# Kernel optimization log

Hardware: AMD Instinct MI355X
Metric: run time of the kernel (lower is better)

Reference implementation:

```python
import jax, jax.numpy as jnp
import numpy as np

D_MODEL = 768
N_HEADS = 4
HEAD_DIM = D_MODEL // N_HEADS


def setup_inputs() -> dict:
    key = jax.random.key(0)
    ks = jax.random.split(key, 9)
    B, S = 4, 2048
    scale = 1.0 / np.sqrt(D_MODEL)
    inputs = jax.random.normal(ks[0], (B, S, D_MODEL), dtype=jnp.float32)
    # Linear weights stored as [in, out] for x @ W + b
    Wq = jax.random.normal(ks[1], (D_MODEL, D_MODEL), dtype=jnp.float32) * scale
    bq = jnp.zeros((D_MODEL,), dtype=jnp.float32)
    Wk = jax.random.normal(ks[2], (D_MODEL, D_MODEL), dtype=jnp.float32) * scale
    bk = jnp.zeros((D_MODEL,), dtype=jnp.float32)
    Wv = jax.random.normal(ks[3], (D_MODEL, D_MODEL), dtype=jnp.float32) * scale
    bv = jnp.zeros((D_MODEL,), dtype=jnp.float32)
    Wo = jax.random.normal(ks[4], (D_MODEL, D_MODEL), dtype=jnp.float32) * scale
    bo = jnp.zeros((D_MODEL,), dtype=jnp.float32)
    return {"inputs": inputs, "Wq": Wq, "bq": bq, "Wk": Wk, "bk": bk,
            "Wv": Wv, "bv": bv, "Wo": Wo, "bo": bo}


def reference(inputs, Wq, bq, Wk, bk, Wv, bv, Wo, bo):
    B, S, _ = inputs.shape
    H, Dh = N_HEADS, HEAD_DIM
    # projections -> [B, H, S, Dh]
    def split_heads(x):
        return x.reshape(B, S, H, Dh).transpose(0, 2, 1, 3)
    Q = split_heads(inputs @ Wq + bq)
    K = split_heads(inputs @ Wk + bk)
    V = split_heads(inputs @ Wv + bv)
    scores = jnp.einsum('bhqd,bhkd->bhqk', Q, K) / jnp.sqrt(jnp.float32(Dh))
    causal = jnp.tril(jnp.ones((S, S), dtype=bool))  # True = keep
    scores = jnp.where(causal, scores, -jnp.inf)
    weights = jax.nn.softmax(scores, axis=-1)
    # dropout is identity in eval mode
    ctx = jnp.einsum('bhqk,bhkd->bhqd', weights, V)
    ctx = ctx.transpose(0, 2, 1, 3).reshape(B, S, H * Dh)
    return ctx @ Wo + bo
```

## Files before the change

### kernel.cpp

```cpp
#include <hip/hip_runtime.h>
#include <hip/hip_bf16.h>
#include <cstddef>

typedef __attribute__((ext_vector_type(8))) short short8;
typedef __attribute__((ext_vector_type(4))) float f32x4;
typedef __attribute__((ext_vector_type(16))) float f32x16;
typedef __attribute__((ext_vector_type(4))) unsigned short u16x4;

#define D_MODEL 768
#define N_HEADS 4
#define HEAD_DIM 192
#define BATCH 4
#define SEQ 2048
#define M_ROWS (BATCH*SEQ)

__device__ __forceinline__ short f2bf(float f) {
  union { float f; unsigned u; } v; v.f = f;
  unsigned r = v.u + 0x7FFFu + ((v.u >> 16) & 1u);
  return (short)(r >> 16);
}

__device__ __forceinline__ float fexp2(float x) {
  return __builtin_amdgcn_exp2f(x);
}

__device__ __forceinline__ void gl_lds16(const void* g, void* l) {
  __builtin_amdgcn_global_load_lds(
      (const __attribute__((address_space(1))) void*)g,
      (__attribute__((address_space(3))) void*)l, 16, 0, 0);
}

__global__ __launch_bounds__(256) void cast_kernel(const float* __restrict__ src,
                                                   short* __restrict__ dst, int n8) {
  int i = blockIdx.x * 256 + threadIdx.x;
  if (i >= n8) return;
  const float4* s = (const float4*)src;
  float4 a = s[2 * i], b = s[2 * i + 1];
  short8 o;
  o[0] = f2bf(a.x); o[1] = f2bf(a.y); o[2] = f2bf(a.z); o[3] = f2bf(a.w);
  o[4] = f2bf(b.x); o[5] = f2bf(b.y); o[6] = f2bf(b.z); o[7] = f2bf(b.w);
  *(short8*)(dst + (size_t)i * 8) = o;
}

__global__ __launch_bounds__(256) void wtrans(const float* __restrict__ W,
                                              short* __restrict__ Wt) {
  __shared__ float tile[32][33];
  int k0 = blockIdx.x * 32, n0 = blockIdx.y * 32;
  int tc = threadIdx.x & 31, tr = threadIdx.x >> 5;
#pragma unroll
  for (int i = 0; i < 4; i++)
    tile[tr + i * 8][tc] = W[(size_t)(k0 + tr + i * 8) * D_MODEL + n0 + tc];
  __syncthreads();
#pragma unroll
  for (int i = 0; i < 4; i++)
    Wt[(size_t)(n0 + tr + i * 8) * D_MODEL + k0 + tc] = f2bf(tile[tc][tr + i * 8]);
}

__global__ __launch_bounds__(256) void bias_concat(const float* __restrict__ a,
                                                   const float* __restrict__ b,
                                                   const float* __restrict__ c,
                                                   float* __restrict__ dst) {
  int i = blockIdx.x * 256 + threadIdx.x;
  if (i >= 3 * D_MODEL) return;
  float v = i < 768 ? a[i] : (i < 1536 ? b[i - 768] : c[i - 1536]);
  dst[i] = v;
}

template <int MODE>
__global__ __launch_bounds__(256, 4) void gemm_bf16(const short* __restrict__ A,
                                                    const short* __restrict__ Wt,
                                                    const float* __restrict__ bias,
                                                    short* __restrict__ oQ,
                                                    short* __restrict__ oK,
                                                    short* __restrict__ oV,
                                                    float* __restrict__ oF, int N) {
  __shared__ short As[128 * 64];
  __shared__ short Bs[128 * 64];
  const int K = 768;
  const int m0 = blockIdx.x * 128, n0 = blockIdx.y * 128;
  const int t = threadIdx.x, lane = t & 63, w = t >> 6;
  const int wr = w >> 1, wc = w & 1, lr = lane & 15, lg = lane >> 4;

  f32x4 acc[4][4] = {};

  for (int k0 = 0; k0 < K; k0 += 64) {
#pragma unroll
    for (int i = 0; i < 4; i++) {
      int id = w * 4 + i;
      int row = id * 8 + (lane >> 3);
      int cc = (lane & 7) ^ (row & 7);
      gl_lds16(A + (size_t)(m0 + row) * K + k0 + cc * 8, As + id * 512);
      gl_lds16(Wt + (size_t)(n0 + row) * K + k0 + cc * 8, Bs + id * 512);
    }
    __syncthreads();
#pragma unroll
    for (int kb = 0; kb < 2; kb++) {
      short8 a[4], b[4];
#pragma unroll
      for (int m = 0; m < 4; m++) {
        int row = wr * 64 + m * 16 + lr;
        a[m] = *(const short8*)&As[row * 64 + (((kb * 4 + lg) ^ (row & 7)) << 3)];
      }
#pragma unroll
      for (int n = 0; n < 4; n++) {
        int row = wc * 64 + n * 16 + lr;
        b[n] = *(const short8*)&Bs[row * 64 + (((kb * 4 + lg) ^ (row & 7)) << 3)];
      }
#pragma unroll
      for (int m = 0; m < 4; m++)
#pragma unroll
        for (int n = 0; n < 4; n++)
          acc[m][n] = __builtin_amdgcn_mfma_f32_16x16x32_bf16(a[m], b[n], acc[m][n], 0, 0, 0);
    }
    __syncthreads();
  }

  if (MODE == 0) {
#pragma unroll
    for (int m = 0; m < 4; m++)
#pragma unroll
      for (int n = 0; n < 4; n++) {
        int col = n0 + wc * 64 + n * 16 + lr;
        float bv = bias[col];
#pragma unroll
        for (int r = 0; r < 4; r++) {
          int row = m0 + wr * 64 + m * 16 + lg * 4 + r;
          oF[(size_t)row * N + col] = acc[m][n][r] + bv;
        }
      }
  } else {
    const int bb = m0 >> 11;
#pragma unroll
    for (int m = 0; m < 4; m++) {
      int s0 = (m0 & (SEQ - 1)) + wr * 64 + m * 16 + lg * 4;
#pragma unroll
      for (int n = 0; n < 4; n++) {
        int col = n0 + wc * 64 + n * 16 + lr;
        int seg = col / 768;
        int d = col - seg * 768;
        int h = d / HEAD_DIM, dd = d - h * HEAD_DIM;
        int bh = bb * N_HEADS + h;
        float bv = bias[col];
        if (seg < 2) {
          short* dst = seg == 0 ? oQ : oK;
#pragma unroll
          for (int r = 0; r < 4; r++)
            dst[((size_t)bh * SEQ + s0 + r) * HEAD_DIM + dd] = f2bf(acc[m][n][r] + bv);
        } else {
          u16x4 pk;
#pragma unroll
          for (int r = 0; r < 4; r++) pk[r] = (unsigned short)f2bf(acc[m][n][r] + bv);
          *(u16x4*)&oV[((size_t)bh * HEAD_DIM + dd) * SEQ + s0] = pk;
        }
      }
    }
  }
}

__device__ __forceinline__ void stage_kv(const short* Kp, const short* Vp, int kbase,
                                         short* KsB, short* VsB, int w, int lane) {
#pragma unroll
  for (int i = 0; i < 6; i++) {
    int id = w * 6 + i;
    int o16 = id * 64 + lane;
    int row = o16 / 24, cc0 = o16 - row * 24;
    int cc = cc0 ^ (row & 7);
    gl_lds16(Kp + (size_t)(kbase + row) * HEAD_DIM + cc * 8, KsB + id * 512);
  }
#pragma unroll
  for (int i = 0; i < 6; i++) {
    int id = w * 6 + i;
    int o16 = id * 64 + lane;
    int row = o16 >> 3, cc = (o16 & 7) ^ (row & 7);
    gl_lds16(Vp + (size_t)row * SEQ + kbase + cc * 8, VsB + id * 512);
  }
}

__global__ __launch_bounds__(256, 2) void attn_kernel(const short* __restrict__ Q,
                                                      const short* __restrict__ Kg,
                                                      const short* __restrict__ Vt,
                                                      short* __restrict__ ctx) {
  __shared__ short smem[64 * 192 + 192 * 64];
  __shared__ float mlbuf[128];
  short* Ks = smem;
  short* Vs = smem + 64 * 192;
  float* obuf = (float*)smem;

  const int i = blockIdx.x;
  int bh, qt;
  if (i < 256) { bh = i & 15; qt = 31 - (i >> 4); }
  else         { int j = i - 256; bh = j & 15; qt = j >> 4; }

  const int b = bh >> 2, head = bh & 3;
  const short* Qp = Q + (size_t)bh * SEQ * HEAD_DIM;
  const short* Kp = Kg + (size_t)bh * SEQ * HEAD_DIM;
  const short* Vp = Vt + (size_t)bh * HEAD_DIM * SEQ;
  const int t = threadIdx.x, lane = t & 63, w = t >> 6;
  const int wq = w >> 1, wk = w & 1;
  const int l31 = lane & 31, hl = lane >> 5;
  const float scale2 = 0.07216878364870322f * 1.4426950408889634f;

  const int nkb = qt + 1;
  const int q0w = qt * 64 + wq * 32;
  const int qlane = q0w + l31;

  short8 qf[12];
#pragma unroll
  for (int c = 0; c < 12; c++)
    qf[c] = *(const short8*)&Qp[(size_t)qlane * HEAD_DIM + c * 16 + hl * 8];

  f32x16 oacc[6];
#pragma unroll
  for (int d = 0; d < 6; d++) oacc[d] = 0.f;
  float m = -3.0e38f, lsum = 0.f;

  for (int kb = 0; kb < nkb; kb++) {
    const int kbase = kb * 64;
    stage_kv(Kp, Vp, kbase, Ks, Vs, w, lane);
    asm volatile("s_waitcnt vmcnt(0)" ::: "memory");
    __builtin_amdgcn_s_barrier();
    asm volatile("" ::: "memory");

    if (kbase + wk * 32 <= q0w + 31) {
      f32x16 sacc = 0.f;
      const int krow = wk * 32 + l31;
      const int krb = krow * 192;
      const int kswz = (krow & 7) << 3;
      __builtin_amdgcn_s_setprio(1);
#pragma unroll
      for (int c = 0; c < 12; c++) {
        short8 kf = *(const short8*)&Ks[krb + ((c * 16 + hl * 8) ^ kswz)];
        sacc = __builtin_amdgcn_mfma_f32_32x32x16_bf16(kf, qf[c], sacc, 0, 0, 0);
      }
      __builtin_amdgcn_s_setprio(0);

      float s[16];
      const bool need_mask = (kbase + wk * 32 + 31) > q0w;
      const int kb0 = kbase + wk * 32 + 4 * hl;
#pragma unroll
      for (int r = 0; r < 16; r++) {
        float v = sacc[r] * scale2;
        if (need_mask) {
          int kg = kb0 + (r & 3) + 8 * (r >> 2);
          if (kg > qlane) v = -3.0e38f;
        }
        s[r] = v;
      }
      float mx = s[0];
#pragma unroll
      for (int r = 1; r < 16; r++) mx = fmaxf(mx, s[r]);
      mx = fmaxf(mx, __shfl_xor(mx, 32, 64));
      if (!__all(mx <= m + 8.0f)) {
        float mn = fmaxf(m, mx);
        float al = fexp2(m - mn);
        m = mn;
        lsum *= al;
#pragma unroll
        for (int d = 0; d < 6; d++) oacc[d] *= al;
      }
      float pr[16];
      float rs = 0.f;
#pragma unroll
      for (int r = 0; r < 16; r++) {
        pr[r] = fexp2(s[r] - m);
        rs += pr[r];
      }
      rs += __shfl_xor(rs, 32, 64);
      lsum += rs;

      unsigned pk[8], ex[8];
#pragma unroll
      for (int j = 0; j < 8; j++) {
        unsigned r0;
        asm("v_cvt_pk_bf16_f32 %0, %1, %2" : "=v"(r0) : "v"(pr[2 * j]), "v"(pr[2 * j + 1]));
        pk[j] = r0;
      }
#pragma unroll
      for (int j = 0; j < 8; j++) ex[j] = __shfl_xor((int)pk[j], 32, 64);
      union { unsigned u[4]; short8 s8; } f0, f1;
      f0.u[0] = hl ? ex[2] : pk[0];
      f0.u[1] = hl ? ex[3] : pk[1];
      f0.u[2] = hl ? pk[2] : ex[0];
      f0.u[3] = hl ? pk[3] : ex[1];
      f1.u[0] = hl ? ex[6] : pk[4];
      f1.u[1] = hl ? ex[7] : pk[5];
      f1.u[2] = hl ? pk[6] : ex[4];
      f1.u[3] = hl ? pk[7] : ex[5];

      __builtin_amdgcn_s_setprio(1);
#pragma unroll
      for (int db = 0; db < 6; db++) {
        const int vrow = db * 32 + l31;
        const int vrb = vrow * 64;
        const int vswz = (vrow & 7) << 3;
        short8 va = *(const short8*)&Vs[vrb + ((wk * 32 + hl * 8) ^ vswz)];
        oacc[db] = __builtin_amdgcn_mfma_f32_32x32x16_bf16(va, f0.s8, oacc[db], 0, 0, 0);
        short8 vb = *(const short8*)&Vs[vrb + ((wk * 32 + 16 + hl * 8) ^ vswz)];
        oacc[db] = __builtin_amdgcn_mfma_f32_32x32x16_bf16(vb, f1.s8, oacc[db], 0, 0, 0);
      }
      __builtin_amdgcn_s_setprio(0);
    }
    asm volatile("" ::: "memory");
    __builtin_amdgcn_s_barrier();
  }

  __syncthreads();
  if (wk == 1) {
    if (lane < 32) {
      mlbuf[wq * 64 + lane] = m;
      mlbuf[wq * 64 + 32 + lane] = lsum;
    }
#pragma unroll
    for (int db = 0; db < 6; db++)
#pragma unroll
      for (int g = 0; g < 4; g++) {
        int d = db * 32 + 8 * g + 4 * hl;
        f32x4 vv;
        vv[0] = oacc[db][4 * g];
        vv[1] = oacc[db][4 * g + 1];
        vv[2] = oacc[db][4 * g + 2];
        vv[3] = oacc[db][4 * g + 3];
        *(f32x4*)&obuf[(wq * 32 + l31) * 192 + (d ^ ((l31 & 7) << 2))] = vv;
      }
  }
  __syncthreads();
  if (wk == 0) {
    float m1 = mlbuf[wq * 64 + l31];
    float l1 = mlbuf[wq * 64 + 32 + l31];
    float ms = fmaxf(m, m1);
    float a0 = fexp2(m - ms), a1 = fexp2(m1 - ms);
    float lt = lsum * a0 + l1 * a1;
    float rl = 1.0f / lt;
#pragma unroll
    for (int db = 0; db < 6; db++)
#pragma unroll
      for (int g = 0; g < 4; g++) {
        int d = db * 32 + 8 * g + 4 * hl;
        f32x4 rd = *(const f32x4*)&obuf[(wq * 32 + l31) * 192 + (d ^ ((l31 & 7) << 2))];
        u16x4 pkk;
#pragma unroll
        for (int r2 = 0; r2 < 4; r2++) {
          float v = (oacc[db][4 * g + r2] * a0 + rd[r2] * a1) * rl;
          pkk[r2] = (unsigned short)f2bf(v);
        }
        *(u16x4*)&ctx[((size_t)b * SEQ + qlane) * D_MODEL + head * HEAD_DIM + d] = pkk;
      }
  }
}

extern "C" void kernel_launch(void* const* d_in, const int* in_sizes, int n_in,
                              void* d_out, int out_size, void* d_ws, size_t ws_size,
                              hipStream_t stream) {
  const float* X  = (const float*)d_in[0];
  const float* Wq = (const float*)d_in[1];
  const float* bq = (const float*)d_in[2];
  const float* Wk = (const float*)d_in[3];
  const float* bk = (const float*)d_in[4];
  const float* Wv = (const float*)d_in[5];
  const float* bv = (const float*)d_in[6];
  const float* Wo = (const float*)d_in[7];
  const float* bo = (const float*)d_in[8];

  char* ws = (char*)d_ws;
  const size_t XB = (size_t)M_ROWS * D_MODEL * 2;
  const size_t WQKV = (size_t)3 * D_MODEL * D_MODEL * 2;
  const size_t WB = (size_t)D_MODEL * D_MODEL * 2;

  short* Xb    = (short*)(ws);
  short* Wqkvt = (short*)(ws + XB);
  short* Wot   = (short*)(ws + XB + WQKV);
  float* bqkv  = (float*)(ws + XB + WQKV + WB);
  short* Qb    = (short*)(ws + XB + WQKV + WB + 12288);
  short* Kb    = (short*)(ws + XB + WQKV + WB + 12288 + XB);
  short* Vtb   = (short*)(ws + XB + WQKV + WB + 12288 + 2 * XB);
  short* Cb    = (short*)(ws + XB + WQKV + WB + 12288 + 3 * XB);

  const int n8x = M_ROWS * D_MODEL / 8;
  cast_kernel<<<(n8x + 255) / 256, 256, 0, stream>>>(X, Xb, n8x);
  dim3 tg(24, 24);
  wtrans<<<tg, 256, 0, stream>>>(Wq, Wqkvt);
  wtrans<<<tg, 256, 0, stream>>>(Wk, Wqkvt + (size_t)768 * 768);
  wtrans<<<tg, 256, 0, stream>>>(Wv, Wqkvt + (size_t)2 * 768 * 768);
  wtrans<<<tg, 256, 0, stream>>>(Wo, Wot);
  bias_concat<<<9, 256, 0, stream>>>(bq, bk, bv, bqkv);

  gemm_bf16<1><<<dim3(M_ROWS / 128, 2304 / 128), 256, 0, stream>>>(
      Xb, Wqkvt, bqkv, Qb, Kb, Vtb, nullptr, 2304);

  attn_kernel<<<512, 256, 0, stream>>>(Qb, Kb, Vtb, Cb);

  gemm_bf16<0><<<dim3(M_ROWS / 128, 768 / 128), 256, 0, stream>>>(
      Cb, Wot, bo, nullptr, nullptr, nullptr, (float*)d_out, 768);
}
```

Baseline: 144.7 us.

## Prefetch next K/V tile into registers to overlap global loads with compute

Replaces the direct global-to-LDS K/V staging with a register-staged software pipeline. The next tile is loaded into registers while the current tile is computed, then written to LDS at the start of the next iteration. The aim is to hide global memory latency behind the MFMA work instead of waiting on vmcnt(0) each iteration. In exchange it costs 12 extra short8 registers per thread, which may reduce occupancy under launch_bounds(256,2), and it adds explicit LDS writes.

```diff
diff --git a/kernel.cpp b/kernel.cpp
--- a/kernel.cpp
+++ b/kernel.cpp
@@ -157,22 +157,25 @@
   }
 }
 
-__device__ __forceinline__ void stage_kv(const short* Kp, const short* Vp, int kbase,
-                                         short* KsB, short* VsB, int w, int lane) {
+__device__ __forceinline__ void load_kv_regs(const short* Kp, const short* Vp, int kbase,
+                                             int w, int lane, short8* kr, short8* vr) {
 #pragma unroll
   for (int i = 0; i < 6; i++) {
-    int id = w * 6 + i;
-    int o16 = id * 64 + lane;
-    int row = o16 / 24, cc0 = o16 - row * 24;
-    int cc = cc0 ^ (row & 7);
-    gl_lds16(Kp + (size_t)(kbase + row) * HEAD_DIM + cc * 8, KsB + id * 512);
-  }
+    int o16 = (w * 6 + i) * 64 + lane;
+    int row = o16 / 24, cc = (o16 - row * 24) ^ (row & 7);
+    kr[i] = *(const short8*)&Kp[(size_t)(kbase + row) * HEAD_DIM + cc * 8];
+    int vrow = o16 >> 3, vcc = (o16 & 7) ^ (vrow & 7);
+    vr[i] = *(const short8*)&Vp[(size_t)vrow * SEQ + kbase + vcc * 8];
+  }
+}
+
+__device__ __forceinline__ void write_kv_lds(short* Ks, short* Vs, int w, int lane,
+                                             const short8* kr, const short8* vr) {
 #pragma unroll
   for (int i = 0; i < 6; i++) {
-    int id = w * 6 + i;
-    int o16 = id * 64 + lane;
-    int row = o16 >> 3, cc = (o16 & 7) ^ (row & 7);
-    gl_lds16(Vp + (size_t)row * SEQ + kbase + cc * 8, VsB + id * 512);
+    int o16 = (w * 6 + i) * 64 + lane;
+    *(short8*)&Ks[o16 * 8] = kr[i];
+    *(short8*)&Vs[o16 * 8] = vr[i];
   }
 }
 
@@ -214,10 +217,20 @@
   for (int d = 0; d < 6; d++) oacc[d] = 0.f;
   float m = -3.0e38f, lsum = 0.f;
 
+  short8 kr[6], vr[6];
+  load_kv_regs(Kp, Vp, 0, w, lane, kr, vr);
+
   for (int kb = 0; kb < nkb; kb++) {
     const int kbase = kb * 64;
-    stage_kv(Kp, Vp, kbase, Ks, Vs, w, lane);
-    asm volatile("s_waitcnt vmcnt(0)" ::: "memory");
+
+    asm volatile("" ::: "memory");
+    __builtin_amdgcn_s_barrier();
+    asm volatile("" ::: "memory");
+    write_kv_lds(Ks, Vs, w, lane, kr, vr);
+    if (kb + 1 < nkb)
+      load_kv_regs(Kp, Vp, kbase + 64, w, lane, kr, vr);
+    asm volatile("s_waitcnt lgkmcnt(0)" ::: "memory");
+    __builtin_amdgcn_sched_barrier(0);
     __builtin_amdgcn_s_barrier();
     asm volatile("" ::: "memory");
 
@@ -300,8 +313,6 @@
       }
       __builtin_amdgcn_s_setprio(0);
     }
-    asm volatile("" ::: "memory");
-    __builtin_amdgcn_s_barrier();
   }
 
   __syncthreads();
```

New measurement: 176.9 us. 1.22x slower.

## Double-buffer K tiles and overlap V loading with QK^T compute

Applied to the files above, without the earlier changes.

Splits K/V staging so the next K tile is prefetched into a second LDS buffer while the current tile is used. The V load for the current block is issued first, and the QK^T MFMAs plus softmax run before waiting on V. A second wait and barrier is placed before the PV matmul. This is meant to hide global-to-LDS latency behind compute. In exchange, LDS per block grows from 48KB to 72KB and each iteration gains an extra barrier, which may limit occupancy.

```diff
diff --git a/kernel.cpp b/kernel.cpp
--- a/kernel.cpp
+++ b/kernel.cpp
@@ -157,16 +157,19 @@
   }
 }
 
-__device__ __forceinline__ void stage_kv(const short* Kp, const short* Vp, int kbase,
-                                         short* KsB, short* VsB, int w, int lane) {
+__device__ __forceinline__ void stage_K(const short* Kp, int kbase, short* KsB,
+                                        int w, int lane) {
 #pragma unroll
   for (int i = 0; i < 6; i++) {
     int id = w * 6 + i;
     int o16 = id * 64 + lane;
-    int row = o16 / 24, cc0 = o16 - row * 24;
-    int cc = cc0 ^ (row & 7);
+    int row = o16 / 24, cc = (o16 - row * 24) ^ (row & 7);
     gl_lds16(Kp + (size_t)(kbase + row) * HEAD_DIM + cc * 8, KsB + id * 512);
   }
+}
+
+__device__ __forceinline__ void stage_V(const short* Vp, int kbase, short* VsB,
+                                        int w, int lane) {
 #pragma unroll
   for (int i = 0; i < 6; i++) {
     int id = w * 6 + i;
@@ -180,10 +183,11 @@
                                                       const short* __restrict__ Kg,
                                                       const short* __restrict__ Vt,
                                                       short* __restrict__ ctx) {
-  __shared__ short smem[64 * 192 + 192 * 64];
+  __shared__ short smem[2 * 64 * 192 + 192 * 64];
   __shared__ float mlbuf[128];
-  short* Ks = smem;
-  short* Vs = smem + 64 * 192;
+  short* Kbuf0 = smem;
+  short* Kbuf1 = smem + 64 * 192;
+  short* Vs = smem + 2 * 64 * 192;
   float* obuf = (float*)smem;
 
   const int i = blockIdx.x;
@@ -214,14 +218,29 @@
   for (int d = 0; d < 6; d++) oacc[d] = 0.f;
   float m = -3.0e38f, lsum = 0.f;
 
+  stage_K(Kp, 0, Kbuf0, w, lane);
+
   for (int kb = 0; kb < nkb; kb++) {
+    const int cur = kb & 1;
     const int kbase = kb * 64;
-    stage_kv(Kp, Vp, kbase, Ks, Vs, w, lane);
-    asm volatile("s_waitcnt vmcnt(0)" ::: "memory");
+    short* Kc = cur ? Kbuf1 : Kbuf0;
+    const bool has_next = (kb + 1 < nkb);
+
+    stage_V(Vp, kbase, Vs, w, lane);
+    if (has_next) {
+      stage_K(Kp, kbase + 64, cur ? Kbuf0 : Kbuf1, w, lane);
+      asm volatile("s_waitcnt vmcnt(12)" ::: "memory");
+    } else {
+      asm volatile("s_waitcnt vmcnt(6)" ::: "memory");
+    }
     __builtin_amdgcn_s_barrier();
     asm volatile("" ::: "memory");
 
-    if (kbase + wk * 32 <= q0w + 31) {
+    const bool active = (kbase + wk * 32 <= q0w + 31);
+    unsigned pk[8], ex[8];
+    float pr[16];
+
+    if (active) {
       f32x16 sacc = 0.f;
       const int krow = wk * 32 + l31;
       const int krb = krow * 192;
@@ -229,7 +248,7 @@
       __builtin_amdgcn_s_setprio(1);
 #pragma unroll
       for (int c = 0; c < 12; c++) {
-        short8 kf = *(const short8*)&Ks[krb + ((c * 16 + hl * 8) ^ kswz)];
+        short8 kf = *(const short8*)&Kc[krb + ((c * 16 + hl * 8) ^ kswz)];
         sacc = __builtin_amdgcn_mfma_f32_32x32x16_bf16(kf, qf[c], sacc, 0, 0, 0);
       }
       __builtin_amdgcn_s_setprio(0);
@@ -258,7 +277,6 @@
 #pragma unroll
         for (int d = 0; d < 6; d++) oacc[d] *= al;
       }
-      float pr[16];
       float rs = 0.f;
 #pragma unroll
       for (int r = 0; r < 16; r++) {
@@ -268,7 +286,6 @@
       rs += __shfl_xor(rs, 32, 64);
       lsum += rs;
 
-      unsigned pk[8], ex[8];
 #pragma unroll
       for (int j = 0; j < 8; j++) {
         unsigned r0;
@@ -277,6 +294,14 @@
       }
 #pragma unroll
       for (int j = 0; j < 8; j++) ex[j] = __shfl_xor((int)pk[j], 32, 64);
+    }
+
+    if (has_next) asm volatile("s_waitcnt vmcnt(6)" ::: "memory");
+    else          asm volatile("s_waitcnt vmcnt(0)" ::: "memory");
+    __builtin_amdgcn_s_barrier();
+    asm volatile("" ::: "memory");
+
+    if (active) {
       union { unsigned u[4]; short8 s8; } f0, f1;
       f0.u[0] = hl ? ex[2] : pk[0];
       f0.u[1] = hl ? ex[3] : pk[1];
```

Result: slower. 150.1 us (+3.7%).
